# Performance work log

Measured on AMD Instinct MI355X. Metric: run time of the kernel, lower is better.

## Reference

```python
import jax, jax.numpy as jnp
import numpy as np

B, N, C, ORDER, COORD, K = 2, 4096, 64, 4, 2, 8
EPS = 1e-8
LN_EPS = 1e-6


def _layer_norm(x, scale, bias):
    mu = jnp.mean(x, axis=-1, keepdims=True)
    var = jnp.mean(jnp.square(x - mu), axis=-1, keepdims=True)
    return (x - mu) * jax.lax.rsqrt(var + LN_EPS) * scale + bias


def _multipole(x, positions, W, order_scales, ln_s, ln_b):
    # stability clamping / NaN masking as in the original
    x = jnp.where(jnp.isnan(x), 0.0, jnp.clip(x, -1e6, 1e6))
    p = jnp.where(jnp.isnan(positions), 0.0, jnp.clip(positions, -1e6, 1e6))
    r = jnp.maximum(jnp.linalg.norm(p, axis=-1, keepdims=True), EPS)  # (B,N,1)
    theta = jnp.arctan2(p[..., 1], p[..., 0] + EPS)  # (B,N)
    per_order = []
    for o in range(ORDER + 1):
        r_o = r ** o
        radial = jnp.tanh(r_o / (1.0 + r_o))          # (B,N,1)
        angular = jnp.cos(o * theta)                    # (B,N)
        mc = x * radial * angular[..., None]            # (B,N,C)
        nm = mc / (jnp.linalg.norm(mc, axis=-1, keepdims=True) + EPS)
        scale = jnp.clip(order_scales[o], 0.01, 1.0)
        per_order.append(nm * scale / (o + 1.0))
    M = jnp.stack(per_order, axis=-1)  # (B,N,C,O+1) per-order weighted moments
    # per-order linear maps, summed over orders (evident intent of (C,C,O+1) weights)
    transformed = jnp.einsum('bnio,ijo->bnj', M, W)
    normalized = _layer_norm(transformed, ln_s, ln_b)
    return jnp.where(jnp.isnan(normalized), x, normalized)


def _local_messages(x, positions, W1, b1, W2, b2):
    # full pairwise distances, then kNN (exclude self)
    d = jnp.linalg.norm(positions[:, :, None, :] - positions[:, None, :, :], axis=-1)  # (B,N,N)
    _, idx = jax.lax.top_k(-d, K + 1)
    nbr = idx[:, :, 1:]  # (B,N,K)
    # gather neighbor features without materializing (B,N,N,C)
    nbr_feat = jax.vmap(lambda xb, ib: xb[ib])(x, nbr)           # (B,N,K,C)
    self_feat = jnp.broadcast_to(x[:, :, None, :], nbr_feat.shape)
    comb = jnp.concatenate([self_feat, nbr_feat], axis=-1)       # (B,N,K,2C)
    msg = jax.nn.gelu(comb @ W1 + b1) @ W2 + b2                  # (B,N,K,C)
    return jnp.mean(msg, axis=2)


def reference(x, positions, multipole_weights, order_scales, mp_ln_scale, mp_ln_bias,
              msg_W1, msg_b1, msg_W2, msg_b2, upd_W1, upd_b1, upd_W2, upd_b2,
              out_ln_scale, out_ln_bias):
    mp = _multipole(x, positions, multipole_weights, order_scales, mp_ln_scale, mp_ln_bias)
    lm = _local_messages(x, positions, msg_W1, msg_b1, msg_W2, msg_b2)
    u = jnp.concatenate([mp, lm], axis=-1)                       # (B,N,2C)
    upd = jax.nn.gelu(u @ upd_W1 + upd_b1) @ upd_W2 + upd_b2     # (B,N,C)
    return _layer_norm(x + upd, out_ln_scale, out_ln_bias)


def setup_inputs() -> dict:
    key = jax.random.key(0)
    ks = jax.random.split(key, 8)
    C2 = 2 * C
    xav = lambda k, shp: jax.random.normal(k, shp) * np.float32(np.sqrt(2.0 / (shp[0] + shp[-1])))
    return {
        'x': jax.random.normal(ks[0], (B, N, C), dtype=jnp.float32),
        'positions': jax.random.normal(ks[1], (B, N, COORD), dtype=jnp.float32),
        'multipole_weights': jax.random.normal(ks[2], (C, C, ORDER + 1)) * np.float32(0.1 / np.sqrt(ORDER + 1) * np.sqrt(1.0 / C)),
        'order_scales': jnp.ones(ORDER + 1) * 0.1,
        'mp_ln_scale': jnp.ones(C), 'mp_ln_bias': jnp.zeros(C),
        'msg_W1': xav(ks[3], (C2, C)), 'msg_b1': jnp.zeros(C),
        'msg_W2': xav(ks[4], (C, C)), 'msg_b2': jnp.zeros(C),
        'upd_W1': xav(ks[5], (C2, C2)), 'upd_b1': jnp.zeros(C2),
        'upd_W2': xav(ks[6], (C2, C)), 'upd_b2': jnp.zeros(C),
        'out_ln_scale': jnp.ones(C), 'out_ln_bias': jnp.zeros(C),
    }
```

## Files before the change

kernel.cpp:

```cpp
#include <hip/hip_runtime.h>
#include <math.h>

#define NNODES 4096
#define KNN 8
#define GX 64
#define NCELL (GX * GX)
#define BOX_LO (-4.5f)
#define CELL_INV (7.11111111f)

__device__ __forceinline__ int binf(float v) {
    int k = (int)floorf((v - BOX_LO) * CELL_INV);
    return min(GX - 1, max(0, k));
}

__device__ __forceinline__ float cleanf(float v) {
    if (v != v) return 0.0f;
    return fminf(fmaxf(v, -1.0e6f), 1.0e6f);
}

__device__ __forceinline__ float gelu_tanh(float v) {
    float v3 = v * v * v;
    float t = tanhf(0.7978845608028654f * (v + 0.044715f * v3));
    return 0.5f * v * (1.0f + t);
}

__device__ __forceinline__ float wave_sum64(float v) {
    #pragma unroll
    for (int off = 32; off > 0; off >>= 1)
        v += __shfl_xor(v, off, 64);
    return v;
}

__global__ __launch_bounds__(1024) void prep_kernel(
    const float* __restrict__ pos, float4* __restrict__ spk,
    int* __restrict__ boff)
{
    __shared__ int cnt[NCELL];
    __shared__ int wsum[16], wexcl[16];

    int b    = blockIdx.x;
    int t    = threadIdx.x;
    int wid  = t >> 6;
    int lane = t & 63;
    const float2* pb = (const float2*)(pos + (size_t)b * NNODES * 2);

    float qx[4], qy[4];
    int ck[4];
    #pragma unroll
    for (int s = 0; s < 4; ++s) cnt[t + s * 1024] = 0;
    __syncthreads();

    #pragma unroll
    for (int s = 0; s < 4; ++s) {
        float2 p = pb[t + s * 1024];
        qx[s] = cleanf(p.x); qy[s] = cleanf(p.y);
        ck[s] = binf(qy[s]) * GX + binf(qx[s]);
        atomicAdd(&cnt[ck[s]], 1);
    }
    __syncthreads();

    int c0 = cnt[4 * t], c1 = cnt[4 * t + 1], c2 = cnt[4 * t + 2], c3 = cnt[4 * t + 3];
    int s4 = c0 + c1 + c2 + c3;
    int sc = s4;
    #pragma unroll
    for (int off = 1; off < 64; off <<= 1) {
        int o = __shfl_up(sc, off, 64);
        if (lane >= off) sc += o;
    }
    if (lane == 63) wsum[wid] = sc;
    __syncthreads();
    if (t < 16) {
        int v = wsum[t];
        #pragma unroll
        for (int off = 1; off < 16; off <<= 1) {
            int o = __shfl_up(v, off, 64);
            if (t >= off) v += o;
        }
        wexcl[t] = v - wsum[t];
    }
    __syncthreads();
    int base = wexcl[wid] + (sc - s4);
    int* bofb = boff + b * (NCELL + 1);
    bofb[4 * t]     = base;
    bofb[4 * t + 1] = base + c0;
    bofb[4 * t + 2] = base + c0 + c1;
    bofb[4 * t + 3] = base + c0 + c1 + c2;
    if (t == 0) bofb[NCELL] = NNODES;
    cnt[4 * t]     = base;
    cnt[4 * t + 1] = base + c0;
    cnt[4 * t + 2] = base + c0 + c1;
    cnt[4 * t + 3] = base + c0 + c1 + c2;
    __syncthreads();

    #pragma unroll
    for (int s = 0; s < 4; ++s) {
        int p = atomicAdd(&cnt[ck[s]], 1);
        spk[(size_t)b * NNODES + p] =
            make_float4(qx[s], qy[s], __int_as_float(t + s * 1024), 0.0f);
    }
}

#define INSERT8(cur)                                                     \
    {                                                                    \
        unsigned long long c_ = (cur);                                   \
        _Pragma("unroll")                                                \
        for (int q_ = 0; q_ < 8; ++q_) {                                 \
            unsigned long long mn_ = (c_ < best[q_]) ? c_ : best[q_];    \
            c_ = (c_ < best[q_]) ? best[q_] : c_;                        \
            best[q_] = mn_;                                              \
        }                                                                \
    }

__global__ __launch_bounds__(512) void knn_kernel(
    const float* __restrict__ pos, const float4* __restrict__ spk,
    const int* __restrict__ boff, int* __restrict__ nbr)
{
    int wid  = threadIdx.x >> 6;
    int lane = threadIdx.x & 63;
    int row  = blockIdx.x * 8 + wid;
    int b    = row >> 12;
    int i    = row & 4095;

    const float4* sp = spk + (size_t)b * NNODES;
    const int*    bo = boff + b * (NCELL + 1);

    float2 pr = ((const float2*)(pos + (size_t)b * NNODES * 2))[i];
    float qx = cleanf(pr.x), qy = cleanf(pr.y);
    int qcx = binf(qx), qcy = binf(qy);

    unsigned long long best[8];
    #pragma unroll
    for (int q = 0; q < 8; ++q) best[q] = ~0ull;

    auto sweep = [&](int s0, int s1) {
        for (int p0 = s0; p0 < s1; p0 += 64) {
            int p = p0 + lane;
            bool valid = (p < s1);
            float4 cp = sp[min(p, s1 - 1)];
            int ci = __float_as_int(cp.z);
            float dx = qx - cp.x, dy = qy - cp.y;
            float d2 = __fadd_rn(__fmul_rn(dx, dx), __fmul_rn(dy, dy));
            unsigned long long cur =
                ((unsigned long long)__float_as_uint(d2) << 32) | (unsigned)ci;
            if (!valid || ci == i) cur = ~0ull;
            INSERT8(cur);
        }
    };

    int r = 1, cxL, cxH, cyL, cyH;
    for (;;) {
        cxL = max(qcx - r, 0); cxH = min(qcx + r, GX - 1);
        cyL = max(qcy - r, 0); cyH = min(qcy + r, GX - 1);
        int cnt = 0;
        for (int cy = cyL; cy <= cyH; ++cy)
            cnt += bo[cy * GX + cxH + 1] - bo[cy * GX + cxL];
        if (cnt >= 9 || (cxL == 0 && cxH == GX - 1 && cyL == 0 && cyH == GX - 1))
            break;
        r += (r < 4) ? 1 : (r >> 1);
    }
    for (int cy = cyL; cy <= cyH; ++cy)
        sweep(bo[cy * GX + cxL], bo[cy * GX + cxH + 1]);

    unsigned long long m8[8];
    #pragma unroll
    for (int rr = 0; rr < 8; ++rr) {
        unsigned long long k = best[0];
        #pragma unroll
        for (int off = 32; off > 0; off >>= 1) {
            unsigned long long o = __shfl_xor(k, off, 64);
            k = (o < k) ? o : k;
        }
        m8[rr] = k;
        if (best[0] == k) {
            #pragma unroll
            for (int q = 0; q < 7; ++q) best[q] = best[q + 1];
            best[7] = ~0ull;
        }
    }

    float U = __uint_as_float((unsigned)(m8[7] >> 32));
    float w = sqrtf(U) * 1.0001f + 1.0e-5f;
    int bxlo = binf(qx - w), bxhi = binf(qx + w);
    int bylo = binf(qy - w), byhi = binf(qy + w);

    #pragma unroll
    for (int q = 0; q < 8; ++q) best[q] = ~0ull;
    unsigned long long inj = m8[0];
    #pragma unroll
    for (int rr = 1; rr < 8; ++rr) inj = (lane == rr) ? m8[rr] : inj;
    if (lane < 8) best[0] = inj;

    for (int cy = bylo; cy <= byhi; ++cy) {
        int rl = bo[cy * GX + bxlo], rh = bo[cy * GX + bxhi + 1];
        if (cy >= cyL && cy <= cyH) {
            int e = bo[cy * GX + min(cxL, bxhi + 1)];
            sweep(rl, e);
            int s = bo[cy * GX + max(cxH + 1, bxlo)];
            sweep(s, rh);
        } else {
            sweep(rl, rh);
        }
    }

    unsigned out_j = 0;
    #pragma unroll
    for (int rr = 0; rr < 8; ++rr) {
        unsigned long long k = best[0];
        #pragma unroll
        for (int off = 32; off > 0; off >>= 1) {
            unsigned long long o = __shfl_xor(k, off, 64);
            k = (o < k) ? o : k;
        }
        if (lane == rr) out_j = (unsigned)k;
        if (best[0] == k) {
            #pragma unroll
            for (int q = 0; q < 7; ++q) best[q] = best[q + 1];
            best[7] = ~0ull;
        }
    }
    if (lane < 8) nbr[(size_t)row * KNN + lane] = (int)out_j;
}

__global__ __launch_bounds__(512) void multipole_gemm_kernel(
    const float* __restrict__ x, const float* __restrict__ pos,
    const float* __restrict__ W, const float* __restrict__ W1,
    const float* __restrict__ osc,
    const float* __restrict__ lns, const float* __restrict__ lnb,
    float* __restrict__ mp, float* __restrict__ ab)
{
    __shared__ float Wl[5][64][64];
    __shared__ float W1l[128][64];
    __shared__ float xsh[32][65];
    __shared__ float xr[32][64];
    __shared__ float csh[32][5];
    int base = blockIdx.x * 32;

    for (int g = threadIdx.x; g < 5 * 64 * 64; g += 512) {
        int o = g % 5; int t = g / 5;
        Wl[o][t >> 6][t & 63] = W[g];
    }
    for (int g = threadIdx.x; g < 128 * 64; g += 512) ((float*)W1l)[g] = W1[g];
    for (int g = threadIdx.x; g < 32 * 64; g += 512) {
        float v = x[(size_t)base * 64 + g];
        xr[g >> 6][g & 63]  = v;
        xsh[g >> 6][g & 63] = cleanf(v);
    }
    __syncthreads();

    if (threadIdx.x < 32) {
        int t = threadIdx.x;
        float ss = 0.0f;
        for (int i = 0; i < 64; ++i) { float v = xsh[t][i]; ss += v * v; }
        float nx = sqrtf(ss);
        int node = base + t;
        float px = cleanf(pos[(size_t)node * 2]);
        float py = cleanf(pos[(size_t)node * 2 + 1]);
        float r = fmaxf(sqrtf(px * px + py * py), 1.0e-8f);
        float th = atan2f(py, px + 1.0e-8f);
        float r2 = r * r, r3 = r2 * r, r4 = r2 * r2;
        float ro[5] = {1.0f, r, r2, r3, r4};
        #pragma unroll
        for (int o = 0; o < 5; ++o) {
            float radial = tanhf(ro[o] / (1.0f + ro[o]));
            float ang = cosf((float)o * th);
            float s = radial * ang;
            float denom = fabsf(s) * nx + 1.0e-8f;
            float sc = fminf(fmaxf(osc[o], 0.01f), 1.0f);
            csh[t][o] = (s / denom) * sc / (float)(o + 1);
        }
    }
    __syncthreads();

    int w = threadIdx.x >> 6;
    int lane = threadIdx.x & 63;
    int nl0 = w * 4;

    float acc[4][5];
    float accA[4] = {0.f, 0.f, 0.f, 0.f};
    float accB[4] = {0.f, 0.f, 0.f, 0.f};
    #pragma unroll
    for (int r_ = 0; r_ < 4; ++r_)
        #pragma unroll
        for (int o = 0; o < 5; ++o) acc[r_][o] = 0.0f;

    for (int i = 0; i < 64; ++i) {
        float w0 = Wl[0][i][lane], w1 = Wl[1][i][lane], w2 = Wl[2][i][lane],
              w3 = Wl[3][i][lane], w4 = Wl[4][i][lane];
        float wa = W1l[i][lane];
        float wb = W1l[64 + i][lane];
        #pragma unroll
        for (int r_ = 0; r_ < 4; ++r_) {
            float xi = xsh[nl0 + r_][i];
            acc[r_][0] += xi * w0; acc[r_][1] += xi * w1; acc[r_][2] += xi * w2;
            acc[r_][3] += xi * w3; acc[r_][4] += xi * w4;
            float xv = xr[nl0 + r_][i];
            accA[r_] += xv * wa;
            accB[r_] += xv * wb;
        }
    }

    float lnsv = lns[lane], lnbv = lnb[lane];
    #pragma unroll
    for (int r_ = 0; r_ < 4; ++r_) {
        int node = base + nl0 + r_;
        float tv = csh[nl0 + r_][0] * acc[r_][0] + csh[nl0 + r_][1] * acc[r_][1]
                 + csh[nl0 + r_][2] * acc[r_][2] + csh[nl0 + r_][3] * acc[r_][3]
                 + csh[nl0 + r_][4] * acc[r_][4];
        float mu = wave_sum64(tv) * (1.0f / 64.0f);
        float dv = tv - mu;
        float var = wave_sum64(dv * dv) * (1.0f / 64.0f);
        float o_ = dv * (1.0f / sqrtf(var + 1.0e-6f)) * lnsv + lnbv;
        if (o_ != o_) o_ = xsh[nl0 + r_][lane];
        mp[(size_t)node * 64 + lane] = o_;
        ab[(size_t)node * 128 + lane]      = accA[r_];
        ab[(size_t)node * 128 + 64 + lane] = accB[r_];
    }
}

__global__ __launch_bounds__(512) void msg_upd_kernel(
    const float* __restrict__ x, const float* __restrict__ ab,
    const int* __restrict__ nbr, const float* __restrict__ mp,
    const float* __restrict__ mb1, const float* __restrict__ mW2,
    const float* __restrict__ mb2,
    const float* __restrict__ uW1, const float* __restrict__ ub1,
    const float* __restrict__ uW2, const float* __restrict__ ub2,
    const float* __restrict__ lns, const float* __restrict__ lnb,
    float* __restrict__ out)
{
    __shared__ float W2l[64][64];
    __shared__ float W1u[128][128];
    __shared__ float W2u[128][64];
    __shared__ alignas(16) float hm[8][64];
    __shared__ alignas(16) float ul[8][128];
    __shared__ alignas(16) float hl[8][128];
    int base = blockIdx.x * 32;

    for (int g = threadIdx.x; g < 64 * 64; g += 512)   ((float*)W2l)[g] = mW2[g];
    for (int g = threadIdx.x; g < 128 * 128; g += 512) ((float*)W1u)[g] = uW1[g];
    for (int g = threadIdx.x; g < 128 * 64; g += 512)  ((float*)W2u)[g] = uW2[g];
    __syncthreads();

    int w = threadIdx.x >> 6;
    int lane = threadIdx.x & 63;
    float b1m = mb1[lane], b2m = mb2[lane];
    float b1a = ub1[lane], b1b = ub1[lane + 64], b2u = ub2[lane];
    float lnsv = lns[lane], lnbv = lnb[lane];

    int node0 = base + w * 4;
    const float* abb = ab + (((size_t)(node0 >> 12)) << 12) * 128;
    const int* nb = nbr + (size_t)node0 * 8;

    float bvc[8];
    {
        int nb0[8];
        #pragma unroll
        for (int k = 0; k < 8; ++k) nb0[k] = nb[k];
        #pragma unroll
        for (int k = 0; k < 8; ++k)
            bvc[k] = abb[(size_t)nb0[k] * 128 + 64 + lane];
    }

    #pragma unroll
    for (int t = 0; t < 4; ++t) {
        int node = node0 + t;
        int nbn[8];
        if (t < 3) {
            #pragma unroll
            for (int k = 0; k < 8; ++k) nbn[k] = nb[8 * (t + 1) + k];
        }
        float a  = ab[(size_t)node * 128 + lane];
        float mpv = mp[(size_t)node * 64 + lane];
        float xv  = x[(size_t)node * 64 + lane];

        float hsum = 0.0f;
        #pragma unroll
        for (int k = 0; k < 8; ++k)
            hsum += gelu_tanh(a + bvc[k] + b1m);
        hm[w][lane] = hsum * 0.125f;

        float bvn[8];
        if (t < 3) {
            #pragma unroll
            for (int k = 0; k < 8; ++k)
                bvn[k] = abb[(size_t)nbn[k] * 128 + 64 + lane];
        }

        float o_ = 0.0f;
        for (int h4 = 0; h4 < 64; h4 += 4) {
            float4 hv = *(const float4*)&hm[w][h4];
            o_ += hv.x * W2l[h4][lane] + hv.y * W2l[h4 + 1][lane]
                + hv.z * W2l[h4 + 2][lane] + hv.w * W2l[h4 + 3][lane];
        }

        ul[w][lane]      = mpv;
        ul[w][64 + lane] = o_ + b2m;

        float h1a = 0.0f, h2a = 0.0f;
        for (int i4 = 0; i4 < 128; i4 += 4) {
            float4 uv = *(const float4*)&ul[w][i4];
            h1a += uv.x * W1u[i4][lane]     + uv.y * W1u[i4 + 1][lane]
                 + uv.z * W1u[i4 + 2][lane] + uv.w * W1u[i4 + 3][lane];
            h2a += uv.x * W1u[i4][lane + 64]     + uv.y * W1u[i4 + 1][lane + 64]
                 + uv.z * W1u[i4 + 2][lane + 64] + uv.w * W1u[i4 + 3][lane + 64];
        }
        hl[w][lane]      = gelu_tanh(h1a + b1a);
        hl[w][64 + lane] = gelu_tanh(h2a + b1b);

        float acc = 0.0f;
        for (int h4 = 0; h4 < 128; h4 += 4) {
            float4 hv = *(const float4*)&hl[w][h4];
            acc += hv.x * W2u[h4][lane] + hv.y * W2u[h4 + 1][lane]
                 + hv.z * W2u[h4 + 2][lane] + hv.w * W2u[h4 + 3][lane];
        }
        float pre = xv + acc + b2u;
        float mu = wave_sum64(pre) * (1.0f / 64.0f);
        float dv = pre - mu;
        float var = wave_sum64(dv * dv) * (1.0f / 64.0f);
        out[(size_t)node * 64 + lane] =
            dv * (1.0f / sqrtf(var + 1.0e-6f)) * lnsv + lnbv;

        #pragma unroll
        for (int k = 0; k < 8; ++k) bvc[k] = bvn[k];
    }
}

extern "C" void kernel_launch(void* const* d_in, const int* in_sizes, int n_in,
                              void* d_out, int out_size, void* d_ws, size_t ws_size,
                              hipStream_t stream)
{
    (void)in_sizes; (void)n_in; (void)out_size; (void)ws_size;
    const float* x     = (const float*)d_in[0];
    const float* pos   = (const float*)d_in[1];
    const float* mw    = (const float*)d_in[2];
    const float* osc   = (const float*)d_in[3];
    const float* mplns = (const float*)d_in[4];
    const float* mplnb = (const float*)d_in[5];
    const float* mW1   = (const float*)d_in[6];
    const float* mb1   = (const float*)d_in[7];
    const float* mW2   = (const float*)d_in[8];
    const float* mb2   = (const float*)d_in[9];
    const float* uW1   = (const float*)d_in[10];
    const float* ub1   = (const float*)d_in[11];
    const float* uW2   = (const float*)d_in[12];
    const float* ub2   = (const float*)d_in[13];
    const float* olns  = (const float*)d_in[14];
    const float* olnb  = (const float*)d_in[15];
    float* out = (float*)d_out;

    char* ws = (char*)d_ws;
    int*    nbr  = (int*)ws;
    float*  mp   = (float*)(ws + 262144);
    float*  ab   = (float*)(ws + 262144 + 2097152);
    float4* spk  = (float4*)(ws + 262144 + 2097152 + 4194304);
    int*    boff = (int*)(ws + 262144 + 2097152 + 4194304 + 131072);

    prep_kernel<<<2, 1024, 0, stream>>>(pos, spk, boff);
    knn_kernel<<<1024, 512, 0, stream>>>(pos, spk, boff, nbr);
    multipole_gemm_kernel<<<256, 512, 0, stream>>>(
        x, pos, mw, mW1, osc, mplns, mplnb, mp, ab);
    msg_upd_kernel<<<256, 512, 0, stream>>>(
        x, ab, nbr, mp, mb1, mW2, mb2, uW1, ub1, uW2, ub2, olns, olnb, out);
}
```

Baseline: 89.69 us.

## Pre-transpose weights and broadcast activations via readlane in GEMM kernels

Six extra blocks in the prep kernel transpose all weight matrices into workspace each call, so the GEMM kernels can load padded float4 weight rows from LDS per lane. Activations are kept in registers and broadcast with readlane instead of being staged through shared memory. msg_upd processes its four nodes in batched stages, not one at a time. This trades LDS traffic and bank conflicts for scalar readlane instructions and more register pressure, and it moves the transpose work into the timed prep launch.

Result: slower. 108.0 us (+20.5%).

```diff
diff --git a/kernel.cpp b/kernel.cpp
--- a/kernel.cpp
+++ b/kernel.cpp
@@ -31,12 +31,49 @@
     return v;
 }
 
+__device__ __forceinline__ float rdl(float v, int l) {
+    return __int_as_float(__builtin_amdgcn_readlane(__float_as_int(v), l));
+}
+
 __global__ __launch_bounds__(1024) void prep_kernel(
     const float* __restrict__ pos, float4* __restrict__ spk,
-    int* __restrict__ boff)
+    int* __restrict__ boff,
+    const float* __restrict__ mw,  const float* __restrict__ mW1,
+    const float* __restrict__ mW2, const float* __restrict__ uW1,
+    const float* __restrict__ uW2,
+    float* __restrict__ uW1t, float* __restrict__ uW2t,
+    float* __restrict__ mW2t, float* __restrict__ mWlt,
+    float* __restrict__ mW1tA, float* __restrict__ mW1tB)
 {
     __shared__ int cnt[NCELL];
     __shared__ int wsum[16], wexcl[16];
+
+    if (blockIdx.x >= 2) {
+        int tid = (blockIdx.x - 2) * 1024 + threadIdx.x;
+        const int STEP = 6 * 1024;
+        for (int g = tid; g < 128 * 128; g += STEP) {
+            int j = g >> 7, i = g & 127;
+            uW1t[g] = uW1[i * 128 + j];
+        }
+        for (int g = tid; g < 64 * 128; g += STEP) {
+            int j = g >> 7, h = g & 127;
+            uW2t[g] = uW2[h * 64 + j];
+        }
+        for (int g = tid; g < 64 * 64; g += STEP) {
+            int j = g >> 6, h = g & 63;
+            mW2t[g] = mW2[h * 64 + j];
+        }
+        for (int g = tid; g < 5 * 64 * 64; g += STEP) {
+            int o = g >> 12, rem = g & 4095, j = rem >> 6, i = rem & 63;
+            mWlt[g] = mw[(i * 64 + j) * 5 + o];
+        }
+        for (int g = tid; g < 64 * 64; g += STEP) {
+            int j = g >> 6, i = g & 63;
+            mW1tA[g] = mW1[i * 64 + j];
+            mW1tB[g] = mW1[(64 + i) * 64 + j];
+        }
+        return;
+    }
 
     int b    = blockIdx.x;
     int t    = threadIdx.x;
@@ -223,28 +260,29 @@
 
 __global__ __launch_bounds__(512) void multipole_gemm_kernel(
     const float* __restrict__ x, const float* __restrict__ pos,
-    const float* __restrict__ W, const float* __restrict__ W1,
-    const float* __restrict__ osc,
+    const float* __restrict__ mWlt, const float* __restrict__ mW1tA,
+    const float* __restrict__ mW1tB, const float* __restrict__ osc,
     const float* __restrict__ lns, const float* __restrict__ lnb,
     float* __restrict__ mp, float* __restrict__ ab)
 {
-    __shared__ float Wl[5][64][64];
-    __shared__ float W1l[128][64];
+    __shared__ alignas(16) float Wl[5 * 64 * 68];
+    __shared__ alignas(16) float WA[64 * 68];
+    __shared__ alignas(16) float WB[64 * 68];
     __shared__ float xsh[32][65];
-    __shared__ float xr[32][64];
     __shared__ float csh[32][5];
     int base = blockIdx.x * 32;
 
-    for (int g = threadIdx.x; g < 5 * 64 * 64; g += 512) {
-        int o = g % 5; int t = g / 5;
-        Wl[o][t >> 6][t & 63] = W[g];
-    }
-    for (int g = threadIdx.x; g < 128 * 64; g += 512) ((float*)W1l)[g] = W1[g];
-    for (int g = threadIdx.x; g < 32 * 64; g += 512) {
-        float v = x[(size_t)base * 64 + g];
-        xr[g >> 6][g & 63]  = v;
-        xsh[g >> 6][g & 63] = cleanf(v);
-    }
+    for (int g = threadIdx.x; g < 5 * 64 * 16; g += 512) {
+        int oj = g >> 4, i4 = (g & 15) * 4;
+        *(float4*)&Wl[oj * 68 + i4] = *(const float4*)&mWlt[oj * 64 + i4];
+    }
+    for (int g = threadIdx.x; g < 64 * 16; g += 512) {
+        int j = g >> 4, i4 = (g & 15) * 4;
+        *(float4*)&WA[j * 68 + i4] = *(const float4*)&mW1tA[j * 64 + i4];
+        *(float4*)&WB[j * 68 + i4] = *(const float4*)&mW1tB[j * 64 + i4];
+    }
+    for (int g = threadIdx.x; g < 32 * 64; g += 512)
+        xsh[g >> 6][g & 63] = cleanf(x[(size_t)base * 64 + g]);
     __syncthreads();
 
     if (threadIdx.x < 32) {
@@ -275,6 +313,13 @@
     int lane = threadIdx.x & 63;
     int nl0 = w * 4;
 
+    float xc[4], xw[4];
+    #pragma unroll
+    for (int r_ = 0; r_ < 4; ++r_) {
+        xc[r_] = xsh[nl0 + r_][lane];
+        xw[r_] = x[(size_t)(base + nl0 + r_) * 64 + lane];
+    }
+
     float acc[4][5];
     float accA[4] = {0.f, 0.f, 0.f, 0.f};
     float accB[4] = {0.f, 0.f, 0.f, 0.f};
@@ -283,19 +328,33 @@
         #pragma unroll
         for (int o = 0; o < 5; ++o) acc[r_][o] = 0.0f;
 
-    for (int i = 0; i < 64; ++i) {
-        float w0 = Wl[0][i][lane], w1 = Wl[1][i][lane], w2 = Wl[2][i][lane],
-              w3 = Wl[3][i][lane], w4 = Wl[4][i][lane];
-        float wa = W1l[i][lane];
-        float wb = W1l[64 + i][lane];
-        #pragma unroll
-        for (int r_ = 0; r_ < 4; ++r_) {
-            float xi = xsh[nl0 + r_][i];
-            acc[r_][0] += xi * w0; acc[r_][1] += xi * w1; acc[r_][2] += xi * w2;
-            acc[r_][3] += xi * w3; acc[r_][4] += xi * w4;
-            float xv = xr[nl0 + r_][i];
-            accA[r_] += xv * wa;
-            accB[r_] += xv * wb;
+    for (int i4 = 0; i4 < 64; i4 += 4) {
+        float4 q0 = *(const float4*)&Wl[(0 * 64 + lane) * 68 + i4];
+        float4 q1 = *(const float4*)&Wl[(1 * 64 + lane) * 68 + i4];
+        float4 q2 = *(const float4*)&Wl[(2 * 64 + lane) * 68 + i4];
+        float4 q3 = *(const float4*)&Wl[(3 * 64 + lane) * 68 + i4];
+        float4 q4 = *(const float4*)&Wl[(4 * 64 + lane) * 68 + i4];
+        float4 qa = *(const float4*)&WA[lane * 68 + i4];
+        float4 qb = *(const float4*)&WB[lane * 68 + i4];
+        float w0v[4] = {q0.x, q0.y, q0.z, q0.w};
+        float w1v[4] = {q1.x, q1.y, q1.z, q1.w};
+        float w2v[4] = {q2.x, q2.y, q2.z, q2.w};
+        float w3v[4] = {q3.x, q3.y, q3.z, q3.w};
+        float w4v[4] = {q4.x, q4.y, q4.z, q4.w};
+        float wav[4] = {qa.x, qa.y, qa.z, qa.w};
+        float wbv[4] = {qb.x, qb.y, qb.z, qb.w};
+        #pragma unroll
+        for (int q = 0; q < 4; ++q) {
+            #pragma unroll
+            for (int r_ = 0; r_ < 4; ++r_) {
+                float xi = rdl(xc[r_], i4 + q);
+                float xv = rdl(xw[r_], i4 + q);
+                acc[r_][0] += xi * w0v[q]; acc[r_][1] += xi * w1v[q];
+                acc[r_][2] += xi * w2v[q]; acc[r_][3] += xi * w3v[q];
+                acc[r_][4] += xi * w4v[q];
+                accA[r_] += xv * wav[q];
+                accB[r_] += xv * wbv[q];
+            }
         }
     }
 
@@ -320,24 +379,29 @@
 __global__ __launch_bounds__(512) void msg_upd_kernel(
     const float* __restrict__ x, const float* __restrict__ ab,
     const int* __restrict__ nbr, const float* __restrict__ mp,
-    const float* __restrict__ mb1, const float* __restrict__ mW2,
+    const float* __restrict__ mb1, const float* __restrict__ mW2t,
     const float* __restrict__ mb2,
-    const float* __restrict__ uW1, const float* __restrict__ ub1,
-    const float* __restrict__ uW2, const float* __restrict__ ub2,
+    const float* __restrict__ uW1t, const float* __restrict__ ub1,
+    const float* __restrict__ uW2t, const float* __restrict__ ub2,
     const float* __restrict__ lns, const float* __restrict__ lnb,
     float* __restrict__ out)
 {
-    __shared__ float W2l[64][64];
-    __shared__ float W1u[128][128];
-    __shared__ float W2u[128][64];
-    __shared__ alignas(16) float hm[8][64];
-    __shared__ alignas(16) float ul[8][128];
-    __shared__ alignas(16) float hl[8][128];
-    int base = blockIdx.x * 32;
-
-    for (int g = threadIdx.x; g < 64 * 64; g += 512)   ((float*)W2l)[g] = mW2[g];
-    for (int g = threadIdx.x; g < 128 * 128; g += 512) ((float*)W1u)[g] = uW1[g];
-    for (int g = threadIdx.x; g < 128 * 64; g += 512)  ((float*)W2u)[g] = uW2[g];
+    __shared__ alignas(16) float W1ul[128 * 132];
+    __shared__ alignas(16) float W2ul[64 * 132];
+    __shared__ alignas(16) float W2ml[64 * 68];
+
+    for (int g = threadIdx.x; g < 128 * 32; g += 512) {
+        int j = g >> 5, i4 = (g & 31) * 4;
+        *(float4*)&W1ul[j * 132 + i4] = *(const float4*)&uW1t[j * 128 + i4];
+    }
+    for (int g = threadIdx.x; g < 64 * 32; g += 512) {
+        int j = g >> 5, h4 = (g & 31) * 4;
+        *(float4*)&W2ul[j * 132 + h4] = *(const float4*)&uW2t[j * 128 + h4];
+    }
+    for (int g = threadIdx.x; g < 64 * 16; g += 512) {
+        int j = g >> 4, h4 = (g & 15) * 4;
+        *(float4*)&W2ml[j * 68 + h4] = *(const float4*)&mW2t[j * 64 + h4];
+    }
     __syncthreads();
 
     int w = threadIdx.x >> 6;
@@ -346,81 +410,116 @@
     float b1a = ub1[lane], b1b = ub1[lane + 64], b2u = ub2[lane];
     float lnsv = lns[lane], lnbv = lnb[lane];
 
-    int node0 = base + w * 4;
+    int node0 = blockIdx.x * 32 + w * 4;
     const float* abb = ab + (((size_t)(node0 >> 12)) << 12) * 128;
     const int* nb = nbr + (size_t)node0 * 8;
 
+    float av[4], uav[4], xv[4], hmr[4];
+    #pragma unroll
+    for (int r = 0; r < 4; ++r) {
+        av[r]  = ab[(size_t)(node0 + r) * 128 + lane];
+        uav[r] = mp[(size_t)(node0 + r) * 64 + lane];
+        xv[r]  = x[(size_t)(node0 + r) * 64 + lane];
+    }
+
     float bvc[8];
-    {
-        int nb0[8];
-        #pragma unroll
-        for (int k = 0; k < 8; ++k) nb0[k] = nb[k];
-        #pragma unroll
-        for (int k = 0; k < 8; ++k)
-            bvc[k] = abb[(size_t)nb0[k] * 128 + 64 + lane];
-    }
-
-    #pragma unroll
-    for (int t = 0; t < 4; ++t) {
-        int node = node0 + t;
-        int nbn[8];
-        if (t < 3) {
-            #pragma unroll
-            for (int k = 0; k < 8; ++k) nbn[k] = nb[8 * (t + 1) + k];
-        }
-        float a  = ab[(size_t)node * 128 + lane];
-        float mpv = mp[(size_t)node * 64 + lane];
-        float xv  = x[(size_t)node * 64 + lane];
-
-        float hsum = 0.0f;
-        #pragma unroll
-        for (int k = 0; k < 8; ++k)
-            hsum += gelu_tanh(a + bvc[k] + b1m);
-        hm[w][lane] = hsum * 0.125f;
-
+    #pragma unroll
+    for (int k = 0; k < 8; ++k)
+        bvc[k] = abb[(size_t)nb[k] * 128 + 64 + lane];
+    #pragma unroll
+    for (int r = 0; r < 4; ++r) {
         float bvn[8];
-        if (t < 3) {
+        if (r < 3) {
             #pragma unroll
             for (int k = 0; k < 8; ++k)
-                bvn[k] = abb[(size_t)nbn[k] * 128 + 64 + lane];
-        }
-
-        float o_ = 0.0f;
-        for (int h4 = 0; h4 < 64; h4 += 4) {
-            float4 hv = *(const float4*)&hm[w][h4];
-            o_ += hv.x * W2l[h4][lane] + hv.y * W2l[h4 + 1][lane]
-                + hv.z * W2l[h4 + 2][lane] + hv.w * W2l[h4 + 3][lane];
-        }
-
-        ul[w][lane]      = mpv;
-        ul[w][64 + lane] = o_ + b2m;
-
-        float h1a = 0.0f, h2a = 0.0f;
-        for (int i4 = 0; i4 < 128; i4 += 4) {
-            float4 uv = *(const float4*)&ul[w][i4];
-            h1a += uv.x * W1u[i4][lane]     + uv.y * W1u[i4 + 1][lane]
-                 + uv.z * W1u[i4 + 2][lane] + uv.w * W1u[i4 + 3][lane];
-            h2a += uv.x * W1u[i4][lane + 64]     + uv.y * W1u[i4 + 1][lane + 64]
-                 + uv.z * W1u[i4 + 2][lane + 64] + uv.w * W1u[i4 + 3][lane + 64];
-        }
-        hl[w][lane]      = gelu_tanh(h1a + b1a);
-        hl[w][64 + lane] = gelu_tanh(h2a + b1b);
-
-        float acc = 0.0f;
-        for (int h4 = 0; h4 < 128; h4 += 4) {
-            float4 hv = *(const float4*)&hl[w][h4];
-            acc += hv.x * W2u[h4][lane] + hv.y * W2u[h4 + 1][lane]
-                 + hv.z * W2u[h4 + 2][lane] + hv.w * W2u[h4 + 3][lane];
-        }
-        float pre = xv + acc + b2u;
+                bvn[k] = abb[(size_t)nb[8 * (r + 1) + k] * 128 + 64 + lane];
+        }
+        float hsum = 0.0f;
+        #pragma unroll
+        for (int k = 0; k < 8; ++k)
+            hsum += gelu_tanh(av[r] + bvc[k] + b1m);
+        hmr[r] = hsum * 0.125f;
+        if (r < 3) {
+            #pragma unroll
+            for (int k = 0; k < 8; ++k) bvc[k] = bvn[k];
+        }
+    }
+
+    float o_[4] = {0.f, 0.f, 0.f, 0.f};
+    #pragma unroll
+    for (int h4 = 0; h4 < 64; h4 += 4) {
+        float4 wq = *(const float4*)&W2ml[lane * 68 + h4];
+        #pragma unroll
+        for (int r = 0; r < 4; ++r) {
+            o_[r] += rdl(hmr[r], h4)     * wq.x + rdl(hmr[r], h4 + 1) * wq.y
+                   + rdl(hmr[r], h4 + 2) * wq.z + rdl(hmr[r], h4 + 3) * wq.w;
+        }
+    }
+    float ubv[4];
+    #pragma unroll
+    for (int r = 0; r < 4; ++r) ubv[r] = o_[r] + b2m;
+
+    float h1a[4] = {0.f, 0.f, 0.f, 0.f}, h2a[4] = {0.f, 0.f, 0.f, 0.f};
+    #pragma unroll
+    for (int i4 = 0; i4 < 64; i4 += 4) {
+        float4 w1 = *(const float4*)&W1ul[lane * 132 + i4];
+        float4 w2 = *(const float4*)&W1ul[(lane + 64) * 132 + i4];
+        #pragma unroll
+        for (int r = 0; r < 4; ++r) {
+            float u0 = rdl(uav[r], i4),     u1 = rdl(uav[r], i4 + 1),
+                  u2 = rdl(uav[r], i4 + 2), u3 = rdl(uav[r], i4 + 3);
+            h1a[r] += u0 * w1.x + u1 * w1.y + u2 * w1.z + u3 * w1.w;
+            h2a[r] += u0 * w2.x + u1 * w2.y + u2 * w2.z + u3 * w2.w;
+        }
+    }
+    #pragma unroll
+    for (int i4 = 0; i4 < 64; i4 += 4) {
+        float4 w1 = *(const float4*)&W1ul[lane * 132 + 64 + i4];
+        float4 w2 = *(const float4*)&W1ul[(lane + 64) * 132 + 64 + i4];
+        #pragma unroll
+        for (int r = 0; r < 4; ++r) {
+            float u0 = rdl(ubv[r], i4),     u1 = rdl(ubv[r], i4 + 1),
+                  u2 = rdl(ubv[r], i4 + 2), u3 = rdl(ubv[r], i4 + 3);
+            h1a[r] += u0 * w1.x + u1 * w1.y + u2 * w1.z + u3 * w1.w;
+            h2a[r] += u0 * w2.x + u1 * w2.y + u2 * w2.z + u3 * w2.w;
+        }
+    }
+
+    float hla[4], hlb[4], accq[4];
+    #pragma unroll
+    for (int r = 0; r < 4; ++r) {
+        hla[r] = gelu_tanh(h1a[r] + b1a);
+        hlb[r] = gelu_tanh(h2a[r] + b1b);
+        accq[r] = 0.f;
+    }
+
+    #pragma unroll
+    for (int h4 = 0; h4 < 64; h4 += 4) {
+        float4 wq = *(const float4*)&W2ul[lane * 132 + h4];
+        #pragma unroll
+        for (int r = 0; r < 4; ++r) {
+            accq[r] += rdl(hla[r], h4)     * wq.x + rdl(hla[r], h4 + 1) * wq.y
+                     + rdl(hla[r], h4 + 2) * wq.z + rdl(hla[r], h4 + 3) * wq.w;
+        }
+    }
+    #pragma unroll
+    for (int h4 = 0; h4 < 64; h4 += 4) {
+        float4 wq = *(const float4*)&W2ul[lane * 132 + 64 + h4];
+        #pragma unroll
+        for (int r = 0; r < 4; ++r) {
+            accq[r] += rdl(hlb[r], h4)     * wq.x + rdl(hlb[r], h4 + 1) * wq.y
+                     + rdl(hlb[r], h4 + 2) * wq.z + rdl(hlb[r], h4 + 3) * wq.w;
+        }
+    }
+
+    #pragma unroll
+    for (int r = 0; r < 4; ++r) {
+        float pre = xv[r] + accq[r] + b2u;
         float mu = wave_sum64(pre) * (1.0f / 64.0f);
         float dv = pre - mu;
         float var = wave_sum64(dv * dv) * (1.0f / 64.0f);
-        out[(size_t)node * 64 + lane] =
+        out[(size_t)(node0 + r) * 64 + lane] =
             dv * (1.0f / sqrtf(var + 1.0e-6f)) * lnsv + lnbv;
-
-        #pragma unroll
-        for (int k = 0; k < 8; ++k) bvc[k] = bvn[k];
     }
 }
 
@@ -448,16 +547,23 @@
     float* out = (float*)d_out;
 
     char* ws = (char*)d_ws;
-    int*    nbr  = (int*)ws;
-    float*  mp   = (float*)(ws + 262144);
-    float*  ab   = (float*)(ws + 262144 + 2097152);
-    float4* spk  = (float4*)(ws + 262144 + 2097152 + 4194304);
-    int*    boff = (int*)(ws + 262144 + 2097152 + 4194304 + 131072);
-
-    prep_kernel<<<2, 1024, 0, stream>>>(pos, spk, boff);
+    int*    nbr   = (int*)ws;
+    float*  mp    = (float*)(ws + 262144);
+    float*  ab    = (float*)(ws + 2359296);
+    float4* spk   = (float4*)(ws + 6553600);
+    int*    boff  = (int*)(ws + 6684672);
+    float*  uW1t  = (float*)(ws + 6717696);
+    float*  uW2t  = (float*)(ws + 6783232);
+    float*  mW2t  = (float*)(ws + 6816000);
+    float*  mWlt  = (float*)(ws + 6832384);
+    float*  mW1tA = (float*)(ws + 6914304);
+    float*  mW1tB = (float*)(ws + 6930688);
+
+    prep_kernel<<<8, 1024, 0, stream>>>(pos, spk, boff,
+        mw, mW1, mW2, uW1, uW2, uW1t, uW2t, mW2t, mWlt, mW1tA, mW1tB);
     knn_kernel<<<1024, 512, 0, stream>>>(pos, spk, boff, nbr);
     multipole_gemm_kernel<<<256, 512, 0, stream>>>(
-        x, pos, mw, mW1, osc, mplns, mplnb, mp, ab);
+        x, pos, mWlt, mW1tA, mW1tB, osc, mplns, mplnb, mp, ab);
     msg_upd_kernel<<<256, 512, 0, stream>>>(
-        x, ab, nbr, mp, mb1, mW2, mb2, uW1, ub1, uW2, ub2, olns, olnb, out);
-}
+        x, ab, nbr, mp, mb1, mW2t, mb2, uW1t, ub1, uW2t, ub2, olns, olnb, out);
+}
```

## Pre-transpose multipole weights in prep kernel and use float4 LDS reads in GEMM

Applied to the files above, without the earlier changes.

Six extra blocks in the prep kernel transpose the multipole weights and msg_W1 into a per-output-column layout in workspace. The multipole GEMM kernel then stages them into padded (stride 68) shared memory with float4 copies and reads four input features per load in the inner loop, replacing the strided mod-5 gather and scalar LDS reads. This is meant to cut shared-memory instruction count and the cost of the gather-style weight load. It adds a small global write/read round trip and more shared memory per block, which may lower occupancy.

New measurement: 88.42 us. Within noise of the previous version (-1.4%).

```diff
diff --git a/kernel.cpp b/kernel.cpp
--- a/kernel.cpp
+++ b/kernel.cpp
@@ -33,10 +33,28 @@
 
 __global__ __launch_bounds__(1024) void prep_kernel(
     const float* __restrict__ pos, float4* __restrict__ spk,
-    int* __restrict__ boff)
+    int* __restrict__ boff,
+    const float* __restrict__ mw,  const float* __restrict__ mW1,
+    float* __restrict__ mWlt, float* __restrict__ mW1tA,
+    float* __restrict__ mW1tB)
 {
     __shared__ int cnt[NCELL];
     __shared__ int wsum[16], wexcl[16];
+
+    if (blockIdx.x >= 2) {
+        int tid = (blockIdx.x - 2) * 1024 + threadIdx.x;
+        const int STEP = 6 * 1024;
+        for (int g = tid; g < 5 * 64 * 64; g += STEP) {
+            int o = g >> 12, rem = g & 4095, j = rem >> 6, i = rem & 63;
+            mWlt[g] = mw[(i * 64 + j) * 5 + o];
+        }
+        for (int g = tid; g < 64 * 64; g += STEP) {
+            int j = g >> 6, i = g & 63;
+            mW1tA[g] = mW1[i * 64 + j];
+            mW1tB[g] = mW1[(64 + i) * 64 + j];
+        }
+        return;
+    }
 
     int b    = blockIdx.x;
     int t    = threadIdx.x;
@@ -223,23 +241,28 @@
 
 __global__ __launch_bounds__(512) void multipole_gemm_kernel(
     const float* __restrict__ x, const float* __restrict__ pos,
-    const float* __restrict__ W, const float* __restrict__ W1,
-    const float* __restrict__ osc,
+    const float* __restrict__ mWlt, const float* __restrict__ mW1tA,
+    const float* __restrict__ mW1tB, const float* __restrict__ osc,
     const float* __restrict__ lns, const float* __restrict__ lnb,
     float* __restrict__ mp, float* __restrict__ ab)
 {
-    __shared__ float Wl[5][64][64];
-    __shared__ float W1l[128][64];
-    __shared__ float xsh[32][65];
-    __shared__ float xr[32][64];
+    __shared__ alignas(16) float Wl[5 * 64 * 68];
+    __shared__ alignas(16) float WA[64 * 68];
+    __shared__ alignas(16) float WB[64 * 68];
+    __shared__ alignas(16) float xsh[32][68];
+    __shared__ alignas(16) float xr[32][68];
     __shared__ float csh[32][5];
     int base = blockIdx.x * 32;
 
-    for (int g = threadIdx.x; g < 5 * 64 * 64; g += 512) {
-        int o = g % 5; int t = g / 5;
-        Wl[o][t >> 6][t & 63] = W[g];
-    }
-    for (int g = threadIdx.x; g < 128 * 64; g += 512) ((float*)W1l)[g] = W1[g];
+    for (int g = threadIdx.x; g < 5 * 64 * 16; g += 512) {
+        int oj = g >> 4, i4 = (g & 15) * 4;
+        *(float4*)&Wl[oj * 68 + i4] = *(const float4*)&mWlt[oj * 64 + i4];
+    }
+    for (int g = threadIdx.x; g < 64 * 16; g += 512) {
+        int j = g >> 4, i4 = (g & 15) * 4;
+        *(float4*)&WA[j * 68 + i4] = *(const float4*)&mW1tA[j * 64 + i4];
+        *(float4*)&WB[j * 68 + i4] = *(const float4*)&mW1tB[j * 64 + i4];
+    }
     for (int g = threadIdx.x; g < 32 * 64; g += 512) {
         float v = x[(size_t)base * 64 + g];
         xr[g >> 6][g & 63]  = v;
@@ -283,21 +306,32 @@
         #pragma unroll
         for (int o = 0; o < 5; ++o) acc[r_][o] = 0.0f;
 
-    for (int i = 0; i < 64; ++i) {
-        float w0 = Wl[0][i][lane], w1 = Wl[1][i][lane], w2 = Wl[2][i][lane],
-              w3 = Wl[3][i][lane], w4 = Wl[4][i][lane];
-        float wa = W1l[i][lane];
-        float wb = W1l[64 + i][lane];
+    #define MG_FMA(R, XI, XV, QC)                                          \
+        { float xi_ = (XI), xv_ = (XV);                                    \
+          acc[R][0] += xi_ * q0.QC; acc[R][1] += xi_ * q1.QC;              \
+          acc[R][2] += xi_ * q2.QC; acc[R][3] += xi_ * q3.QC;              \
+          acc[R][4] += xi_ * q4.QC;                                        \
+          accA[R] += xv_ * qa.QC;  accB[R] += xv_ * qb.QC; }
+
+    for (int i4 = 0; i4 < 64; i4 += 4) {
+        float4 q0 = *(const float4*)&Wl[(0 * 64 + lane) * 68 + i4];
+        float4 q1 = *(const float4*)&Wl[(1 * 64 + lane) * 68 + i4];
+        float4 q2 = *(const float4*)&Wl[(2 * 64 + lane) * 68 + i4];
+        float4 q3 = *(const float4*)&Wl[(3 * 64 + lane) * 68 + i4];
+        float4 q4 = *(const float4*)&Wl[(4 * 64 + lane) * 68 + i4];
+        float4 qa = *(const float4*)&WA[lane * 68 + i4];
+        float4 qb = *(const float4*)&WB[lane * 68 + i4];
         #pragma unroll
         for (int r_ = 0; r_ < 4; ++r_) {
-            float xi = xsh[nl0 + r_][i];
-            acc[r_][0] += xi * w0; acc[r_][1] += xi * w1; acc[r_][2] += xi * w2;
-            acc[r_][3] += xi * w3; acc[r_][4] += xi * w4;
-            float xv = xr[nl0 + r_][i];
-            accA[r_] += xv * wa;
-            accB[r_] += xv * wb;
-        }
-    }
+            float4 xc4 = *(const float4*)&xsh[nl0 + r_][i4];
+            float4 xw4 = *(const float4*)&xr[nl0 + r_][i4];
+            MG_FMA(r_, xc4.x, xw4.x, x)
+            MG_FMA(r_, xc4.y, xw4.y, y)
+            MG_FMA(r_, xc4.z, xw4.z, z)
+            MG_FMA(r_, xc4.w, xw4.w, w)
+        }
+    }
+    #undef MG_FMA
 
     float lnsv = lns[lane], lnbv = lnb[lane];
     #pragma unroll
@@ -448,16 +482,20 @@
     float* out = (float*)d_out;
 
     char* ws = (char*)d_ws;
-    int*    nbr  = (int*)ws;
-    float*  mp   = (float*)(ws + 262144);
-    float*  ab   = (float*)(ws + 262144 + 2097152);
-    float4* spk  = (float4*)(ws + 262144 + 2097152 + 4194304);
-    int*    boff = (int*)(ws + 262144 + 2097152 + 4194304 + 131072);
-
-    prep_kernel<<<2, 1024, 0, stream>>>(pos, spk, boff);
+    int*    nbr   = (int*)ws;
+    float*  mp    = (float*)(ws + 262144);
+    float*  ab    = (float*)(ws + 2359296);
+    float4* spk   = (float4*)(ws + 6553600);
+    int*    boff  = (int*)(ws + 6684672);
+    float*  mWlt  = (float*)(ws + 6721536);
+    float*  mW1tA = (float*)(ws + 6803456);
+    float*  mW1tB = (float*)(ws + 6819840);
+
+    prep_kernel<<<8, 1024, 0, stream>>>(pos, spk, boff,
+        mw, mW1, mWlt, mW1tA, mW1tB);
     knn_kernel<<<1024, 512, 0, stream>>>(pos, spk, boff, nbr);
     multipole_gemm_kernel<<<256, 512, 0, stream>>>(
-        x, pos, mw, mW1, osc, mplns, mplnb, mp, ab);
+        x, pos, mWlt, mW1tA, mW1tB, osc, mplns, mplnb, mp, ab);
     msg_upd_kernel<<<256, 512, 0, stream>>>(
         x, ab, nbr, mp, mb1, mW2, mb2, uW1, ub1, uW2, ub2, olns, olnb, out);
 }
```
